# Kernel optimization log

Hardware: AMD Instinct MI355X
Metric: run time of the kernel (lower is better)

The kernel has to match this reference:

```python
import math
import jax, jax.numpy as jnp
import numpy as np

B, S, D, H = 2, 2048, 2048, 16
HD = D // H
SCALE = 1.0 / math.sqrt(HD)


def setup_inputs() -> dict:
    key = jax.random.key(0)
    kx, kq, kk, kv, ko = jax.random.split(key, 5)
    w_std = 1.0 / math.sqrt(D)
    return {
        "x": jax.random.normal(kx, (B, S, D), jnp.float32),
        "Wq": jax.random.normal(kq, (D, D), jnp.float32) * w_std,
        "Wk": jax.random.normal(kk, (D, D), jnp.float32) * w_std,
        "Wv": jax.random.normal(kv, (D, D), jnp.float32) * w_std,
        "Wo": jax.random.normal(ko, (D, D), jnp.float32) * w_std,
        "attention_mask": jnp.ones((B, S), jnp.int32),
        "sliding_window": 512,
        "sink_tokens": 4,
    }


def reference(x, Wq, Wk, Wv, Wo, attention_mask, sliding_window, sink_tokens):
    b, s, d = x.shape
    # nn.Linear(bias=False): y = x @ W^T
    q = (x @ Wq.T).reshape(b, s, H, HD).transpose(0, 2, 1, 3)  # [b,h,s,hd]
    k = (x @ Wk.T).reshape(b, s, H, HD).transpose(0, 2, 1, 3)
    v = (x @ Wv.T).reshape(b, s, H, HD).transpose(0, 2, 1, 3)

    scores = jnp.einsum("bhqd,bhkd->bhqk", q, k) * SCALE  # [b,h,s,s]

    i = jnp.arange(s)[:, None]
    j = jnp.arange(s)[None, :]
    causal = j <= i
    window = (j >= i - sliding_window + 1) & (j <= i)
    # sink mask in the source fills [0:i+1] for every row (rows < sink_tokens
    # and rows >= sink_tokens alike), i.e. it is identical to the causal mask.
    sink = causal
    allowed = causal & window & sink  # [s,s]
    pad = (attention_mask != 0)[:, None, None, :]  # [b,1,1,s]
    scores = jnp.where(allowed[None, None] & pad, scores, -jnp.inf)

    attn = jax.nn.softmax(scores, axis=-1)
    out = jnp.einsum("bhqk,bhkd->bhqd", attn, v)  # [b,h,s,hd]
    out = out.transpose(0, 2, 1, 3).reshape(b, s, d)
    return out @ Wo.T
```

## Files before the change

### kernel.cpp

```cpp
#include <hip/hip_runtime.h>
#include <stdint.h>


typedef __attribute__((ext_vector_type(8))) short short8;
typedef __attribute__((ext_vector_type(4))) float f32x4;

#define DEV static __device__ __forceinline__

DEV unsigned short f2bf(float f) {
  unsigned u = __builtin_bit_cast(unsigned, f);
  u += 0x7fffu + ((u >> 16) & 1u);
  return (unsigned short)(u >> 16);
}

DEV void async16(const void* g, void* l) {
  __builtin_amdgcn_global_load_lds(
      (const __attribute__((address_space(1))) unsigned int*)g,
      (__attribute__((address_space(3))) unsigned int*)l, 16, 0, 0);
}

__global__ void cast_bf16(const float* __restrict__ src,
                          unsigned short* __restrict__ dst, int n8) {
  int i = blockIdx.x * blockDim.x + threadIdx.x;
  if (i >= n8) return;
  const float4* s4 = (const float4*)src;
  float4 a = s4[2 * (size_t)i], b = s4[2 * (size_t)i + 1];
  short8 o;
  o[0] = (short)f2bf(a.x); o[1] = (short)f2bf(a.y);
  o[2] = (short)f2bf(a.z); o[3] = (short)f2bf(a.w);
  o[4] = (short)f2bf(b.x); o[5] = (short)f2bf(b.y);
  o[6] = (short)f2bf(b.z); o[7] = (short)f2bf(b.w);
  *(short8*)(dst + 8 * (size_t)i) = o;
}

constexpr int GM = 4096, GN = 2048, GK = 2048;

template <bool STORE_BF16>
__global__ __launch_bounds__(256) void gemm_bt(
    const unsigned short* __restrict__ A, const unsigned short* __restrict__ B,
    void* __restrict__ Cout) {
  __shared__ short As[128 * 32];
  __shared__ short Bs[128 * 32];
  const int t = threadIdx.x;
  const int wave = t >> 6, lane = t & 63;
  const int row0 = blockIdx.x * 128, col0 = blockIdx.y * 128;
  const int wrow = (wave >> 1) * 64, wcol = (wave & 1) * 64;

  f32x4 acc[4][4] = {};

  const int srow = wave * 16 + (lane >> 2);
  const int cg = (lane & 3) ^ (lane >> 4);
  const unsigned short* Ag0 = A + (size_t)(row0 + srow) * GK + cg * 8;
  const unsigned short* Ag1 = A + (size_t)(row0 + 64 + srow) * GK + cg * 8;
  const unsigned short* Bg0 = B + (size_t)(col0 + srow) * GK + cg * 8;
  const unsigned short* Bg1 = B + (size_t)(col0 + 64 + srow) * GK + cg * 8;
  char* lA0 = (char*)As + wave * 1024;
  char* lA1 = (char*)As + 4096 + wave * 1024;
  char* lB0 = (char*)Bs + wave * 1024;
  char* lB1 = (char*)Bs + 4096 + wave * 1024;

  const int quad = lane >> 4, l15 = lane & 15;
  const int cpos = quad ^ ((l15 >> 2) & 3);
  const short* ap[4];
  const short* bp[4];
#pragma unroll
  for (int i = 0; i < 4; ++i) {
    ap[i] = As + (wrow + i * 16 + l15) * 32 + cpos * 8;
    bp[i] = Bs + (wcol + i * 16 + l15) * 32 + cpos * 8;
  }

  for (int kk = 0; kk < GK; kk += 32) {
    async16(Ag0 + kk, lA0);
    async16(Ag1 + kk, lA1);
    async16(Bg0 + kk, lB0);
    async16(Bg1 + kk, lB1);
    __syncthreads();
    short8 af[4], bf[4];
#pragma unroll
    for (int i = 0; i < 4; ++i) af[i] = *(const short8*)ap[i];
#pragma unroll
    for (int i = 0; i < 4; ++i) bf[i] = *(const short8*)bp[i];
#pragma unroll
    for (int mi = 0; mi < 4; ++mi)
#pragma unroll
      for (int ni = 0; ni < 4; ++ni)
        acc[mi][ni] = __builtin_amdgcn_mfma_f32_16x16x32_bf16(
            af[mi], bf[ni], acc[mi][ni], 0, 0, 0);
    __syncthreads();
  }

#pragma unroll
  for (int mi = 0; mi < 4; ++mi)
#pragma unroll
    for (int ni = 0; ni < 4; ++ni)
#pragma unroll
      for (int r = 0; r < 4; ++r) {
        int row = row0 + wrow + mi * 16 + quad * 4 + r;
        int col = col0 + wcol + ni * 16 + l15;
        if (STORE_BF16)
          ((unsigned short*)Cout)[(size_t)row * GN + col] = f2bf(acc[mi][ni][r]);
        else
          ((float*)Cout)[(size_t)row * GN + col] = acc[mi][ni][r];
      }
}

__global__ __launch_bounds__(256) void transpose_v(
    const unsigned short* __restrict__ vb, unsigned short* __restrict__ vtb) {
  __shared__ unsigned short tile[64][72];
  const int s0 = blockIdx.x * 64, d0 = blockIdx.y * 64, b = blockIdx.z;
  const int tid = threadIdx.x;
  const int c8 = tid & 7;
#pragma unroll
  for (int i = 0; i < 2; ++i) {
    int row = i * 32 + (tid >> 3);
    uint4 v = *(const uint4*)(vb + (size_t)(b * 2048 + s0 + row) * 2048 + d0 + c8 * 8);
    *(uint4*)&tile[row][c8 * 8] = v;
  }
  __syncthreads();
#pragma unroll
  for (int i = 0; i < 2; ++i) {
    int dr = i * 32 + (tid >> 3);
    short8 sv;
#pragma unroll
    for (int j = 0; j < 8; ++j) sv[j] = (short)tile[c8 * 8 + j][dr];
    int d = d0 + dr;
    int h = d >> 7, hd = d & 127;
    *(short8*)(vtb + ((size_t)(b * 16 + h) * 128 + hd) * 2048 + s0 + c8 * 8) = sv;
  }
}

__global__ __launch_bounds__(256, 3) void attn_mfma(
    const unsigned short* __restrict__ Qm, const unsigned short* __restrict__ Km,
    const unsigned short* __restrict__ Vt, unsigned short* __restrict__ Om,
    const int* __restrict__ amask, const int* __restrict__ winp) {
  constexpr int S = 2048, D = 2048, HD = 128;
  const float SCALE = 0.08838834764831845f;

  __shared__ short Ks[64 * 128];
  __shared__ short Vts[128 * 64];
  __shared__ short Ps[4][16 * 64];

  const int t = threadIdx.x, w = t >> 6, lane = t & 63;
  const int quad = lane >> 4, l15 = lane & 15;
  const int l7 = l15 & 7;
  const int qt = blockIdx.x, h = blockIdx.y, b = blockIdx.z;
  const int qi0 = qt * 64;
  const int win = winp[0];

  short8 qf[4];
  {
    const unsigned short* qp =
        Qm + (size_t)(b * S + qi0 + w * 16 + l15) * D + h * HD + quad * 8;
#pragma unroll
    for (int kc = 0; kc < 4; ++kc) qf[kc] = *(const short8*)(qp + kc * 32);
  }

  f32x4 o[8] = {};
  float m_r[4], l_r[4];
#pragma unroll
  for (int r = 0; r < 4; ++r) { m_r[r] = -1e30f; l_r[r] = 0.f; }

  int lowj = qi0 - win + 1;
  if (lowj < 0) lowj = 0;
  const int jt0 = lowj >> 6;

  const int krow = lane >> 4, kpos = lane & 15;
  const int vrow = lane >> 3, vpos = lane & 7;

  for (int jt = jt0; jt <= qt; ++jt) {
    const int j0 = jt * 64;
    __syncthreads();
#pragma unroll
    for (int ii = 0; ii < 4; ++ii) {
      int row = ii * 16 + w * 4 + krow;
      int c = kpos ^ (row & 7);
      async16(Km + (size_t)(b * S + j0 + row) * D + h * HD + c * 8,
              (char*)Ks + (ii * 16 + w * 4) * 256);
    }
#pragma unroll
    for (int ii = 0; ii < 4; ++ii) {
      int row = ii * 32 + w * 8 + vrow;
      int c = vpos ^ (row & 7);
      async16(Vt + ((size_t)(b * 16 + h) * 128 + row) * S + j0 + c * 8,
              (char*)Vts + (ii * 32 + w * 8) * 128);
    }
    __syncthreads();

    f32x4 sS[4];
#pragma unroll
    for (int ni = 0; ni < 4; ++ni) {
      f32x4 acc = {0.f, 0.f, 0.f, 0.f};
#pragma unroll
      for (int kc = 0; kc < 4; ++kc) {
        int pos = (kc * 4 + quad) ^ l7;
        short8 bk = *(const short8*)&Ks[(ni * 16 + l15) * 128 + pos * 8];
        acc = __builtin_amdgcn_mfma_f32_16x16x32_bf16(qf[kc], bk, acc, 0, 0, 0);
      }
      sS[ni] = acc;
    }

    float sv[4][4];
    int amv[4];
#pragma unroll
    for (int ni = 0; ni < 4; ++ni) amv[ni] = amask[b * S + j0 + ni * 16 + l15];
#pragma unroll
    for (int ni = 0; ni < 4; ++ni)
#pragma unroll
      for (int r = 0; r < 4; ++r) {
        int gi = qi0 + w * 16 + quad * 4 + r;
        int gj = j0 + ni * 16 + l15;
        bool ok = (gj <= gi) && (gj >= gi - win + 1) && (amv[ni] != 0);
        sv[ni][r] = ok ? sS[ni][r] * SCALE : -1e30f;
      }
    float alpha[4], mnew[4];
#pragma unroll
    for (int r = 0; r < 4; ++r) {
      float mx = fmaxf(fmaxf(sv[0][r], sv[1][r]), fmaxf(sv[2][r], sv[3][r]));
      mx = fmaxf(mx, __shfl_xor(mx, 1));
      mx = fmaxf(mx, __shfl_xor(mx, 2));
      mx = fmaxf(mx, __shfl_xor(mx, 4));
      mx = fmaxf(mx, __shfl_xor(mx, 8));
      float mn = fmaxf(m_r[r], mx);
      alpha[r] = __expf(m_r[r] - mn);
      m_r[r] = mn;
      mnew[r] = mn;
    }
    float rs[4] = {0.f, 0.f, 0.f, 0.f};
#pragma unroll
    for (int ni = 0; ni < 4; ++ni)
#pragma unroll
      for (int r = 0; r < 4; ++r) {
        float p = (sv[ni][r] > -1e29f) ? __expf(sv[ni][r] - mnew[r]) : 0.f;
        sv[ni][r] = p;
        rs[r] += p;
      }
#pragma unroll
    for (int r = 0; r < 4; ++r) {
      float s = rs[r];
      s += __shfl_xor(s, 1);
      s += __shfl_xor(s, 2);
      s += __shfl_xor(s, 4);
      s += __shfl_xor(s, 8);
      l_r[r] = l_r[r] * alpha[r] + s;
    }
#pragma unroll
    for (int ni = 0; ni < 4; ++ni)
#pragma unroll
      for (int r = 0; r < 4; ++r) {
        int row = quad * 4 + r;
        int col = ni * 16 + l15;
        int pos = (col >> 3) ^ (row & 7);
        Ps[w][row * 64 + pos * 8 + (col & 7)] = (short)f2bf(sv[ni][r]);
      }
#pragma unroll
    for (int ni2 = 0; ni2 < 8; ++ni2)
#pragma unroll
      for (int r = 0; r < 4; ++r) o[ni2][r] *= alpha[r];

    __asm__ __volatile__("s_waitcnt lgkmcnt(0)" ::: "memory");

    short8 aP[2];
#pragma unroll
    for (int kc2 = 0; kc2 < 2; ++kc2) {
      int pos = (kc2 * 4 + quad) ^ l7;
      aP[kc2] = *(const short8*)&Ps[w][l15 * 64 + pos * 8];
    }
#pragma unroll
    for (int ni2 = 0; ni2 < 8; ++ni2) {
#pragma unroll
      for (int kc2 = 0; kc2 < 2; ++kc2) {
        int pos = (kc2 * 4 + quad) ^ l7;
        short8 bv = *(const short8*)&Vts[(ni2 * 16 + l15) * 64 + pos * 8];
        o[ni2] = __builtin_amdgcn_mfma_f32_16x16x32_bf16(aP[kc2], bv, o[ni2], 0, 0, 0);
      }
    }
  }

  float inv[4];
#pragma unroll
  for (int r = 0; r < 4; ++r) inv[r] = 1.f / l_r[r];
#pragma unroll
  for (int ni2 = 0; ni2 < 8; ++ni2)
#pragma unroll
    for (int r = 0; r < 4; ++r) {
      int row = qi0 + w * 16 + quad * 4 + r;
      Om[(size_t)(b * S + row) * D + h * HD + ni2 * 16 + l15] =
          f2bf(o[ni2][r] * inv[r]);
    }
}

extern "C" void kernel_launch(void* const* d_in, const int* in_sizes, int n_in,
                              void* d_out, int out_size, void* d_ws,
                              size_t ws_size, hipStream_t stream) {
  (void)in_sizes; (void)n_in; (void)out_size; (void)ws_size;
  const float* x  = (const float*)d_in[0];
  const float* Wq = (const float*)d_in[1];
  const float* Wk = (const float*)d_in[2];
  const float* Wv = (const float*)d_in[3];
  const float* Wo = (const float*)d_in[4];
  const int* am   = (const int*)d_in[5];
  const int* win  = (const int*)d_in[6];

  char* ws = (char*)d_ws;
  unsigned short* xb  = (unsigned short*)(ws + 0);
  unsigned short* vtb = (unsigned short*)(ws + 0);
  unsigned short* wqb = (unsigned short*)(ws + 16777216);
  unsigned short* wkb = (unsigned short*)(ws + 25165824);
  unsigned short* wvb = (unsigned short*)(ws + 33554432);
  unsigned short* wob = (unsigned short*)(ws + 41943040);
  unsigned short* qb  = (unsigned short*)(ws + 50331648);
  unsigned short* kb  = (unsigned short*)(ws + 67108864);
  unsigned short* vb  = (unsigned short*)(ws + 83886080);
  unsigned short* ab  = (unsigned short*)(ws + 100663296);

  cast_bf16<<<dim3(4096), dim3(256), 0, stream>>>(x, xb, 1048576);
  cast_bf16<<<dim3(2048), dim3(256), 0, stream>>>(Wq, wqb, 524288);
  cast_bf16<<<dim3(2048), dim3(256), 0, stream>>>(Wk, wkb, 524288);
  cast_bf16<<<dim3(2048), dim3(256), 0, stream>>>(Wv, wvb, 524288);
  cast_bf16<<<dim3(2048), dim3(256), 0, stream>>>(Wo, wob, 524288);

  gemm_bt<true><<<dim3(32, 16), dim3(256), 0, stream>>>(xb, wqb, qb);
  gemm_bt<true><<<dim3(32, 16), dim3(256), 0, stream>>>(xb, wkb, kb);
  gemm_bt<true><<<dim3(32, 16), dim3(256), 0, stream>>>(xb, wvb, vb);

  transpose_v<<<dim3(32, 32, 2), dim3(256), 0, stream>>>(vb, vtb);

  attn_mfma<<<dim3(32, 16, 2), dim3(256), 0, stream>>>(qb, kb, vtb, ab, am, win);

  gemm_bt<false><<<dim3(32, 16), dim3(256), 0, stream>>>(ab, wob, d_out);
}
```

Measured before the change: 407.5 us.

## Fuse QKV projections into one GEMM launch and double attention query tile

Places the cast Wq, Wk and Wv weights contiguously so one GEMM launch with a tripled N grid computes Q, K and V, routing each output column block to its buffer by stride. The attention kernel now handles 128 query rows per block (32 per wave, two MFMA row tiles), so each loaded K/V tile serves twice as many queries, and waves skip tiles entirely outside their window. The costs are more registers, lowering launch bounds occupancy from 3 to 2 blocks per CU, and half as many attention blocks. Some waves also idle on tiles that only other waves in the block need.

```diff
diff --git a/kernel.cpp b/kernel.cpp
--- a/kernel.cpp
+++ b/kernel.cpp
@@ -33,17 +33,19 @@
   *(short8*)(dst + 8 * (size_t)i) = o;
 }
 
-constexpr int GM = 4096, GN = 2048, GK = 2048;
+constexpr int GK = 2048, GN = 2048;
 
 template <bool STORE_BF16>
 __global__ __launch_bounds__(256) void gemm_bt(
     const unsigned short* __restrict__ A, const unsigned short* __restrict__ B,
-    void* __restrict__ Cout) {
+    void* __restrict__ Cout, size_t obuf_stride) {
   __shared__ short As[128 * 32];
   __shared__ short Bs[128 * 32];
   const int t = threadIdx.x;
   const int wave = t >> 6, lane = t & 63;
-  const int row0 = blockIdx.x * 128, col0 = blockIdx.y * 128;
+  const int row0 = blockIdx.x * 128;
+  const int col0g = blockIdx.y * 128;
+  const int nb = col0g >> 11, col0 = col0g & 2047;
   const int wrow = (wave >> 1) * 64, wcol = (wave & 1) * 64;
 
   f32x4 acc[4][4] = {};
@@ -52,8 +54,8 @@
   const int cg = (lane & 3) ^ (lane >> 4);
   const unsigned short* Ag0 = A + (size_t)(row0 + srow) * GK + cg * 8;
   const unsigned short* Ag1 = A + (size_t)(row0 + 64 + srow) * GK + cg * 8;
-  const unsigned short* Bg0 = B + (size_t)(col0 + srow) * GK + cg * 8;
-  const unsigned short* Bg1 = B + (size_t)(col0 + 64 + srow) * GK + cg * 8;
+  const unsigned short* Bg0 = B + (size_t)(col0g + srow) * GK + cg * 8;
+  const unsigned short* Bg1 = B + (size_t)(col0g + 64 + srow) * GK + cg * 8;
   char* lA0 = (char*)As + wave * 1024;
   char* lA1 = (char*)As + 4096 + wave * 1024;
   char* lB0 = (char*)Bs + wave * 1024;
@@ -98,9 +100,11 @@
         int row = row0 + wrow + mi * 16 + quad * 4 + r;
         int col = col0 + wcol + ni * 16 + l15;
         if (STORE_BF16)
-          ((unsigned short*)Cout)[(size_t)row * GN + col] = f2bf(acc[mi][ni][r]);
+          ((unsigned short*)Cout)[nb * obuf_stride + (size_t)row * GN + col] =
+              f2bf(acc[mi][ni][r]);
         else
-          ((float*)Cout)[(size_t)row * GN + col] = acc[mi][ni][r];
+          ((float*)Cout)[nb * obuf_stride + (size_t)row * GN + col] =
+              acc[mi][ni][r];
       }
 }
 
@@ -129,7 +133,7 @@
   }
 }
 
-__global__ __launch_bounds__(256, 3) void attn_mfma(
+__global__ __launch_bounds__(256, 2) void attn_mfma(
     const unsigned short* __restrict__ Qm, const unsigned short* __restrict__ Km,
     const unsigned short* __restrict__ Vt, unsigned short* __restrict__ Om,
     const int* __restrict__ amask, const int* __restrict__ winp) {
@@ -138,36 +142,40 @@
 
   __shared__ short Ks[64 * 128];
   __shared__ short Vts[128 * 64];
-  __shared__ short Ps[4][16 * 64];
+  __shared__ short Ps[4][2][16 * 64];
 
   const int t = threadIdx.x, w = t >> 6, lane = t & 63;
   const int quad = lane >> 4, l15 = lane & 15;
   const int l7 = l15 & 7;
   const int qt = blockIdx.x, h = blockIdx.y, b = blockIdx.z;
-  const int qi0 = qt * 64;
+  const int qi0 = qt * 128;
   const int win = winp[0];
 
-  short8 qf[4];
-  {
+  short8 qf[2][4];
+#pragma unroll
+  for (int mi = 0; mi < 2; ++mi) {
     const unsigned short* qp =
-        Qm + (size_t)(b * S + qi0 + w * 16 + l15) * D + h * HD + quad * 8;
-#pragma unroll
-    for (int kc = 0; kc < 4; ++kc) qf[kc] = *(const short8*)(qp + kc * 32);
-  }
-
-  f32x4 o[8] = {};
-  float m_r[4], l_r[4];
-#pragma unroll
-  for (int r = 0; r < 4; ++r) { m_r[r] = -1e30f; l_r[r] = 0.f; }
+        Qm + (size_t)(b * S + qi0 + w * 32 + mi * 16 + l15) * D + h * HD + quad * 8;
+#pragma unroll
+    for (int kc = 0; kc < 4; ++kc) qf[mi][kc] = *(const short8*)(qp + kc * 32);
+  }
+
+  f32x4 o[2][8] = {};
+  float m_r[2][4], l_r[2][4];
+#pragma unroll
+  for (int mi = 0; mi < 2; ++mi)
+#pragma unroll
+    for (int r = 0; r < 4; ++r) { m_r[mi][r] = -1e30f; l_r[mi][r] = 0.f; }
 
   int lowj = qi0 - win + 1;
   if (lowj < 0) lowj = 0;
-  const int jt0 = lowj >> 6;
-
+  const int jt0 = lowj >> 6, jt1 = 2 * qt + 1;
+
+  const int gmin = qi0 + w * 32, gmax = gmin + 31;
   const int krow = lane >> 4, kpos = lane & 15;
   const int vrow = lane >> 3, vpos = lane & 7;
 
-  for (int jt = jt0; jt <= qt; ++jt) {
+  for (int jt = jt0; jt <= jt1; ++jt) {
     const int j0 = jt * 64;
     __syncthreads();
 #pragma unroll
@@ -186,107 +194,125 @@
     }
     __syncthreads();
 
-    f32x4 sS[4];
+    if (j0 > gmax || j0 + 63 < gmin - win + 1) continue;
+
+    int amv[4];
+#pragma unroll
+    for (int ni = 0; ni < 4; ++ni) amv[ni] = amask[b * S + j0 + ni * 16 + l15];
+
+    f32x4 sS[2][4];
 #pragma unroll
     for (int ni = 0; ni < 4; ++ni) {
-      f32x4 acc = {0.f, 0.f, 0.f, 0.f};
+      f32x4 a0 = {0.f, 0.f, 0.f, 0.f}, a1 = {0.f, 0.f, 0.f, 0.f};
 #pragma unroll
       for (int kc = 0; kc < 4; ++kc) {
         int pos = (kc * 4 + quad) ^ l7;
         short8 bk = *(const short8*)&Ks[(ni * 16 + l15) * 128 + pos * 8];
-        acc = __builtin_amdgcn_mfma_f32_16x16x32_bf16(qf[kc], bk, acc, 0, 0, 0);
-      }
-      sS[ni] = acc;
+        a0 = __builtin_amdgcn_mfma_f32_16x16x32_bf16(qf[0][kc], bk, a0, 0, 0, 0);
+        a1 = __builtin_amdgcn_mfma_f32_16x16x32_bf16(qf[1][kc], bk, a1, 0, 0, 0);
+      }
+      sS[0][ni] = a0;
+      sS[1][ni] = a1;
     }
 
-    float sv[4][4];
-    int amv[4];
-#pragma unroll
-    for (int ni = 0; ni < 4; ++ni) amv[ni] = amask[b * S + j0 + ni * 16 + l15];
-#pragma unroll
-    for (int ni = 0; ni < 4; ++ni)
+    float alpha[2][4];
+#pragma unroll
+    for (int mi = 0; mi < 2; ++mi) {
+      float sv[4][4];
+#pragma unroll
+      for (int ni = 0; ni < 4; ++ni)
+#pragma unroll
+        for (int r = 0; r < 4; ++r) {
+          int gi = qi0 + w * 32 + mi * 16 + quad * 4 + r;
+          int gj = j0 + ni * 16 + l15;
+          bool ok = (gj <= gi) && (gj >= gi - win + 1) && (amv[ni] != 0);
+          sv[ni][r] = ok ? sS[mi][ni][r] * SCALE : -1e30f;
+        }
+      float mnew[4];
 #pragma unroll
       for (int r = 0; r < 4; ++r) {
-        int gi = qi0 + w * 16 + quad * 4 + r;
-        int gj = j0 + ni * 16 + l15;
-        bool ok = (gj <= gi) && (gj >= gi - win + 1) && (amv[ni] != 0);
-        sv[ni][r] = ok ? sS[ni][r] * SCALE : -1e30f;
-      }
-    float alpha[4], mnew[4];
-#pragma unroll
-    for (int r = 0; r < 4; ++r) {
-      float mx = fmaxf(fmaxf(sv[0][r], sv[1][r]), fmaxf(sv[2][r], sv[3][r]));
-      mx = fmaxf(mx, __shfl_xor(mx, 1));
-      mx = fmaxf(mx, __shfl_xor(mx, 2));
-      mx = fmaxf(mx, __shfl_xor(mx, 4));
-      mx = fmaxf(mx, __shfl_xor(mx, 8));
-      float mn = fmaxf(m_r[r], mx);
-      alpha[r] = __expf(m_r[r] - mn);
-      m_r[r] = mn;
-      mnew[r] = mn;
+        float mx = fmaxf(fmaxf(sv[0][r], sv[1][r]), fmaxf(sv[2][r], sv[3][r]));
+        mx = fmaxf(mx, __shfl_xor(mx, 1));
+        mx = fmaxf(mx, __shfl_xor(mx, 2));
+        mx = fmaxf(mx, __shfl_xor(mx, 4));
+        mx = fmaxf(mx, __shfl_xor(mx, 8));
+        float mn = fmaxf(m_r[mi][r], mx);
+        alpha[mi][r] = __expf(m_r[mi][r] - mn);
+        m_r[mi][r] = mn;
+        mnew[r] = mn;
+      }
+      float rs[4] = {0.f, 0.f, 0.f, 0.f};
+#pragma unroll
+      for (int ni = 0; ni < 4; ++ni)
+#pragma unroll
+        for (int r = 0; r < 4; ++r) {
+          float p = (sv[ni][r] > -1e29f) ? __expf(sv[ni][r] - mnew[r]) : 0.f;
+          sv[ni][r] = p;
+          rs[r] += p;
+        }
+#pragma unroll
+      for (int r = 0; r < 4; ++r) {
+        float s = rs[r];
+        s += __shfl_xor(s, 1);
+        s += __shfl_xor(s, 2);
+        s += __shfl_xor(s, 4);
+        s += __shfl_xor(s, 8);
+        l_r[mi][r] = l_r[mi][r] * alpha[mi][r] + s;
+      }
+#pragma unroll
+      for (int ni = 0; ni < 4; ++ni)
+#pragma unroll
+        for (int r = 0; r < 4; ++r) {
+          int row = quad * 4 + r;
+          int col = ni * 16 + l15;
+          int pos = (col >> 3) ^ (row & 7);
+          Ps[w][mi][row * 64 + pos * 8 + (col & 7)] = (short)f2bf(sv[ni][r]);
+        }
     }
-    float rs[4] = {0.f, 0.f, 0.f, 0.f};
-#pragma unroll
-    for (int ni = 0; ni < 4; ++ni)
-#pragma unroll
-      for (int r = 0; r < 4; ++r) {
-        float p = (sv[ni][r] > -1e29f) ? __expf(sv[ni][r] - mnew[r]) : 0.f;
-        sv[ni][r] = p;
-        rs[r] += p;
-      }
-#pragma unroll
-    for (int r = 0; r < 4; ++r) {
-      float s = rs[r];
-      s += __shfl_xor(s, 1);
-      s += __shfl_xor(s, 2);
-      s += __shfl_xor(s, 4);
-      s += __shfl_xor(s, 8);
-      l_r[r] = l_r[r] * alpha[r] + s;
-    }
-#pragma unroll
-    for (int ni = 0; ni < 4; ++ni)
-#pragma unroll
-      for (int r = 0; r < 4; ++r) {
-        int row = quad * 4 + r;
-        int col = ni * 16 + l15;
-        int pos = (col >> 3) ^ (row & 7);
-        Ps[w][row * 64 + pos * 8 + (col & 7)] = (short)f2bf(sv[ni][r]);
+#pragma unroll
+    for (int mi = 0; mi < 2; ++mi)
+#pragma unroll
+      for (int ni2 = 0; ni2 < 8; ++ni2)
+#pragma unroll
+        for (int r = 0; r < 4; ++r) o[mi][ni2][r] *= alpha[mi][r];
+
+    __asm__ __volatile__("s_waitcnt lgkmcnt(0)" ::: "memory");
+
+    short8 aP[2][2];
+#pragma unroll
+    for (int mi = 0; mi < 2; ++mi)
+#pragma unroll
+      for (int kc2 = 0; kc2 < 2; ++kc2) {
+        int pos = (kc2 * 4 + quad) ^ l7;
+        aP[mi][kc2] = *(const short8*)&Ps[w][mi][l15 * 64 + pos * 8];
       }
 #pragma unroll
     for (int ni2 = 0; ni2 < 8; ++ni2)
-#pragma unroll
-      for (int r = 0; r < 4; ++r) o[ni2][r] *= alpha[r];
-
-    __asm__ __volatile__("s_waitcnt lgkmcnt(0)" ::: "memory");
-
-    short8 aP[2];
-#pragma unroll
-    for (int kc2 = 0; kc2 < 2; ++kc2) {
-      int pos = (kc2 * 4 + quad) ^ l7;
-      aP[kc2] = *(const short8*)&Ps[w][l15 * 64 + pos * 8];
-    }
-#pragma unroll
-    for (int ni2 = 0; ni2 < 8; ++ni2) {
 #pragma unroll
       for (int kc2 = 0; kc2 < 2; ++kc2) {
         int pos = (kc2 * 4 + quad) ^ l7;
         short8 bv = *(const short8*)&Vts[(ni2 * 16 + l15) * 64 + pos * 8];
-        o[ni2] = __builtin_amdgcn_mfma_f32_16x16x32_bf16(aP[kc2], bv, o[ni2], 0, 0, 0);
-      }
-    }
-  }
-
-  float inv[4];
-#pragma unroll
-  for (int r = 0; r < 4; ++r) inv[r] = 1.f / l_r[r];
-#pragma unroll
-  for (int ni2 = 0; ni2 < 8; ++ni2)
-#pragma unroll
-    for (int r = 0; r < 4; ++r) {
-      int row = qi0 + w * 16 + quad * 4 + r;
-      Om[(size_t)(b * S + row) * D + h * HD + ni2 * 16 + l15] =
-          f2bf(o[ni2][r] * inv[r]);
-    }
+        o[0][ni2] = __builtin_amdgcn_mfma_f32_16x16x32_bf16(aP[0][kc2], bv,
+                                                            o[0][ni2], 0, 0, 0);
+        o[1][ni2] = __builtin_amdgcn_mfma_f32_16x16x32_bf16(aP[1][kc2], bv,
+                                                            o[1][ni2], 0, 0, 0);
+      }
+  }
+
+#pragma unroll
+  for (int mi = 0; mi < 2; ++mi) {
+    float inv[4];
+#pragma unroll
+    for (int r = 0; r < 4; ++r) inv[r] = 1.f / l_r[mi][r];
+#pragma unroll
+    for (int ni2 = 0; ni2 < 8; ++ni2)
+#pragma unroll
+      for (int r = 0; r < 4; ++r) {
+        int row = qi0 + w * 32 + mi * 16 + quad * 4 + r;
+        Om[(size_t)(b * S + row) * D + h * HD + ni2 * 16 + l15] =
+            f2bf(o[mi][ni2][r] * inv[r]);
+      }
+  }
 }
 
 extern "C" void kernel_launch(void* const* d_in, const int* in_sizes, int n_in,
@@ -302,30 +328,26 @@
   const int* win  = (const int*)d_in[6];
 
   char* ws = (char*)d_ws;
-  unsigned short* xb  = (unsigned short*)(ws + 0);
-  unsigned short* vtb = (unsigned short*)(ws + 0);
-  unsigned short* wqb = (unsigned short*)(ws + 16777216);
-  unsigned short* wkb = (unsigned short*)(ws + 25165824);
-  unsigned short* wvb = (unsigned short*)(ws + 33554432);
-  unsigned short* wob = (unsigned short*)(ws + 41943040);
-  unsigned short* qb  = (unsigned short*)(ws + 50331648);
-  unsigned short* kb  = (unsigned short*)(ws + 67108864);
-  unsigned short* vb  = (unsigned short*)(ws + 83886080);
-  unsigned short* ab  = (unsigned short*)(ws + 100663296);
+  unsigned short* xb   = (unsigned short*)(ws + 0);
+  unsigned short* vtb  = (unsigned short*)(ws + 0);
+  unsigned short* wqkv = (unsigned short*)(ws + 16777216);
+  unsigned short* wob  = (unsigned short*)(ws + 41943040);
+  unsigned short* qb   = (unsigned short*)(ws + 50331648);
+  unsigned short* kb   = (unsigned short*)(ws + 67108864);
+  unsigned short* vb   = (unsigned short*)(ws + 83886080);
+  unsigned short* ab   = (unsigned short*)(ws + 100663296);
 
   cast_bf16<<<dim3(4096), dim3(256), 0, stream>>>(x, xb, 1048576);
-  cast_bf16<<<dim3(2048), dim3(256), 0, stream>>>(Wq, wqb, 524288);
-  cast_bf16<<<dim3(2048), dim3(256), 0, stream>>>(Wk, wkb, 524288);
-  cast_bf16<<<dim3(2048), dim3(256), 0, stream>>>(Wv, wvb, 524288);
+  cast_bf16<<<dim3(2048), dim3(256), 0, stream>>>(Wq, wqkv, 524288);
+  cast_bf16<<<dim3(2048), dim3(256), 0, stream>>>(Wk, wqkv + 4194304, 524288);
+  cast_bf16<<<dim3(2048), dim3(256), 0, stream>>>(Wv, wqkv + 8388608, 524288);
   cast_bf16<<<dim3(2048), dim3(256), 0, stream>>>(Wo, wob, 524288);
 
-  gemm_bt<true><<<dim3(32, 16), dim3(256), 0, stream>>>(xb, wqb, qb);
-  gemm_bt<true><<<dim3(32, 16), dim3(256), 0, stream>>>(xb, wkb, kb);
-  gemm_bt<true><<<dim3(32, 16), dim3(256), 0, stream>>>(xb, wvb, vb);
+  gemm_bt<true><<<dim3(32, 48), dim3(256), 0, stream>>>(xb, wqkv, qb, 8388608);
 
   transpose_v<<<dim3(32, 32, 2), dim3(256), 0, stream>>>(vb, vtb);
 
-  attn_mfma<<<dim3(32, 16, 2), dim3(256), 0, stream>>>(qb, kb, vtb, ab, am, win);
-
-  gemm_bt<false><<<dim3(32, 16), dim3(256), 0, stream>>>(ab, wob, d_out);
-}
+  attn_mfma<<<dim3(16, 16, 2), dim3(256), 0, stream>>>(qb, kb, vtb, ab, am, win);
+
+  gemm_bt<false><<<dim3(32, 16), dim3(256), 0, stream>>>(ab, wob, d_out, 0);
+}
```

Result: faster. 378.6 us (-7.1%).
